# Kernel optimization log

Measured on AMD Instinct MI355X. Metric: run time of the kernel, lower is better.

Reference implementation:

```python
import jax, jax.numpy as jnp
import numpy as np

BATCH = 262144
NUM_LAYERS = 64


def setup_inputs() -> dict:
    key = jax.random.key(0)
    k1, k2, k3 = jax.random.split(key, 3)
    X = jax.random.normal(k1, (BATCH, 2), dtype=jnp.float32)
    weights = jax.random.normal(k2, (NUM_LAYERS, 3), dtype=jnp.float32)
    biases = jax.random.normal(k3, (NUM_LAYERS, 3), dtype=jnp.float32)
    return {"X": X, "weights": weights, "biases": biases}


def _unitaries(X, weights, biases):
    # Pad data with constant 1 -> [B, 3]
    Xp = jnp.concatenate([X, jnp.ones((X.shape[0], 1), X.dtype)], axis=1)
    # angles[b, k, l] = weights[l, k] * Xp[b, k] + biases[l, k]  -> [B, 3, L]
    angles = Xp[:, :, None] * weights.T[None, :, :] + biases.T[None, :, :]
    phi, theta, omega = angles[:, 0, :], angles[:, 1, :], angles[:, 2, :]  # [B, L]
    ct = jnp.cos(theta / 2)
    st = jnp.sin(theta / 2)
    ppo = (phi + omega) / 2
    pmo = (phi - omega) / 2
    m00 = jnp.exp(-1j * ppo) * ct
    m01 = -jnp.exp(1j * pmo) * st
    m10 = jnp.exp(-1j * pmo) * st
    m11 = jnp.exp(1j * ppo) * ct
    # [B, L, 2, 2] -> [L, B, 2, 2]
    M = jnp.stack([jnp.stack([m00, m01], axis=-1),
                   jnp.stack([m10, m11], axis=-1)], axis=-2)
    return jnp.transpose(M, (1, 0, 2, 3))


def reference(X, weights, biases):
    M = _unitaries(X, weights, biases)  # [L, B, 2, 2] complex64
    B = X.shape[0]
    s0 = jnp.tile(jnp.array([1.0 + 0.0j, 0.0 + 0.0j], dtype=M.dtype), (B, 1))  # |0>

    def step(s, u):  # s: [B, 2], u: [B, 2, 2]
        s = jnp.einsum('bij,bj->bi', u, s)
        return s, s

    _, states = jax.lax.scan(step, s0, M)  # [L, B, 2] complex64
    return states
```

## Files before the change

kernel.cpp:

```cpp
#include <hip/hip_runtime.h>

#define BATCH 262144
#define NUM_LAYERS 64

template <int MODE>
__global__ __launch_bounds__(256) void squbit_kernel(
    const float* __restrict__ X,
    const float* __restrict__ W,
    const float* __restrict__ Bi,
    float* __restrict__ out)
{
    __shared__ float4 c4[NUM_LAYERS];
    __shared__ float  com[NUM_LAYERS];

    const int t = threadIdx.x;
    if (t < NUM_LAYERS) {
        const float w0 = W[t * 3 + 0], w1 = W[t * 3 + 1], w2 = W[t * 3 + 2];
        const float b0 = Bi[t * 3 + 0], b1 = Bi[t * 3 + 1], b2 = Bi[t * 3 + 2];
        c4[t]  = make_float4(0.5f * w0, 0.5f * b0, 0.5f * w1, 0.5f * b1);
        com[t] = 0.5f * (w2 + b2);
    }
    __syncthreads();

    const int b = blockIdx.x * 256 + t;
    const float2 x = *reinterpret_cast<const float2*>(X + 2 * b);

    float s0r = 1.0f, s0i = 0.0f, s1r = 0.0f, s1i = 0.0f;

    float2* o2 = reinterpret_cast<float2*>(out) + b;
    float4* o4 = reinterpret_cast<float4*>(out) + b;

    #pragma unroll 4
    for (int l = 0; l < NUM_LAYERS; ++l) {
        const float4 c  = c4[l];
        const float omh = com[l];

        const float ph  = fmaf(x.x, c.x, c.y);
        const float th  = fmaf(x.y, c.z, c.w);
        const float ppo = ph + omh;
        const float pmo = ph - omh;

        float st, ct, sp, cp, sm, cm;
        __sincosf(th,  &st, &ct);
        __sincosf(ppo, &sp, &cp);
        __sincosf(pmo, &sm, &cm);

        const float m00r =  ct * cp, m00i = -ct * sp;
        const float m01r = -st * cm, m01i = -st * sm;
        const float m10r =  st * cm, m10i = -st * sm;
        const float m11r =  ct * cp, m11i =  ct * sp;

        const float n0r = m00r * s0r - m00i * s0i + m01r * s1r - m01i * s1i;
        const float n0i = m00r * s0i + m00i * s0r + m01r * s1i + m01i * s1r;
        const float n1r = m10r * s0r - m10i * s0i + m11r * s1r - m11i * s1i;
        const float n1i = m10r * s0i + m10i * s0r + m11r * s1i + m11i * s1r;

        s0r = n0r; s0i = n0i; s1r = n1r; s1i = n1i;

        if (MODE == 0) {
            o2[l * BATCH] = make_float2(s0r, s1r);
        } else {
            o4[l * BATCH] = make_float4(s0r, s0i, s1r, s1i);
        }
    }
}

extern "C" void kernel_launch(void* const* d_in, const int* in_sizes, int n_in,
                              void* d_out, int out_size, void* d_ws, size_t ws_size,
                              hipStream_t stream) {
    const float* X  = (const float*)d_in[0];
    const float* W  = (const float*)d_in[1];
    const float* Bi = (const float*)d_in[2];
    float* out = (float*)d_out;

    dim3 grid(BATCH / 256), block(256);

    const long long full_complex_floats = (long long)NUM_LAYERS * BATCH * 4;
    if ((long long)out_size >= full_complex_floats) {
        squbit_kernel<1><<<grid, block, 0, stream>>>(X, W, Bi, out);
    } else {
        squbit_kernel<0><<<grid, block, 0, stream>>>(X, W, Bi, out);
    }
}
```

Baseline: 31.55 us.

## Factor unitary into Rz-Ry-Rz, defer omega phase, process two samples per thread

Rewrites each layer's unitary as Rz(omega)·Ry(theta)·Rz(phi) and folds each layer's trailing omega rotation into the next layer's phi angle. The per-batch sincos count drops from three to two, and the omega rotation becomes a constant sincos computed once per block and applied only when writing the output. Each thread now handles two batch elements, with the grid halved, to add instruction-level parallelism and use wider float4 loads and stores. The cost is higher register pressure, and the folded angle could change floating-point rounding slightly.

Result: faster. 29.04 us (-8.0%).

```diff
diff --git a/kernel.cpp b/kernel.cpp
--- a/kernel.cpp
+++ b/kernel.cpp
@@ -10,57 +10,84 @@
     const float* __restrict__ Bi,
     float* __restrict__ out)
 {
-    __shared__ float4 c4[NUM_LAYERS];
-    __shared__ float  com[NUM_LAYERS];
+    __shared__ float4 cA[NUM_LAYERS];
+    __shared__ float2 cOm[NUM_LAYERS];
 
     const int t = threadIdx.x;
     if (t < NUM_LAYERS) {
         const float w0 = W[t * 3 + 0], w1 = W[t * 3 + 1], w2 = W[t * 3 + 2];
         const float b0 = Bi[t * 3 + 0], b1 = Bi[t * 3 + 1], b2 = Bi[t * 3 + 2];
-        c4[t]  = make_float4(0.5f * w0, 0.5f * b0, 0.5f * w1, 0.5f * b1);
-        com[t] = 0.5f * (w2 + b2);
+        float hom_prev = 0.0f;
+        if (t > 0) hom_prev = 0.5f * (W[(t - 1) * 3 + 2] + Bi[(t - 1) * 3 + 2]);
+        cA[t] = make_float4(0.5f * w0, fmaf(0.5f, b0, hom_prev), 0.5f * w1, 0.5f * b1);
+        const float hom = 0.5f * (w2 + b2);
+        float so, co;
+        __sincosf(hom, &so, &co);
+        cOm[t] = make_float2(co, so);
     }
     __syncthreads();
 
-    const int b = blockIdx.x * 256 + t;
-    const float2 x = *reinterpret_cast<const float2*>(X + 2 * b);
+    const int g = blockIdx.x * 256 + t;
+    const float4 xx = reinterpret_cast<const float4*>(X)[g];
 
-    float s0r = 1.0f, s0i = 0.0f, s1r = 0.0f, s1i = 0.0f;
+    float Aur0 = 1.0f, Aui0 = 0.0f, Aur1 = 0.0f, Aui1 = 0.0f;
+    float Bur0 = 1.0f, Bui0 = 0.0f, Bur1 = 0.0f, Bui1 = 0.0f;
 
-    float2* o2 = reinterpret_cast<float2*>(out) + b;
-    float4* o4 = reinterpret_cast<float4*>(out) + b;
+    float4* o4 = reinterpret_cast<float4*>(out);
 
     #pragma unroll 4
     for (int l = 0; l < NUM_LAYERS; ++l) {
-        const float4 c  = c4[l];
-        const float omh = com[l];
+        const float4 c = cA[l];
+        const float2 om = cOm[l];
 
-        const float ph  = fmaf(x.x, c.x, c.y);
-        const float th  = fmaf(x.y, c.z, c.w);
-        const float ppo = ph + omh;
-        const float pmo = ph - omh;
-
-        float st, ct, sp, cp, sm, cm;
-        __sincosf(th,  &st, &ct);
-        __sincosf(ppo, &sp, &cp);
-        __sincosf(pmo, &sm, &cm);
-
-        const float m00r =  ct * cp, m00i = -ct * sp;
-        const float m01r = -st * cm, m01i = -st * sm;
-        const float m10r =  st * cm, m10i = -st * sm;
-        const float m11r =  ct * cp, m11i =  ct * sp;
-
-        const float n0r = m00r * s0r - m00i * s0i + m01r * s1r - m01i * s1i;
-        const float n0i = m00r * s0i + m00i * s0r + m01r * s1i + m01i * s1r;
-        const float n1r = m10r * s0r - m10i * s0i + m11r * s1r - m11i * s1i;
-        const float n1i = m10r * s0i + m10i * s0r + m11r * s1i + m11i * s1r;
-
-        s0r = n0r; s0i = n0i; s1r = n1r; s1i = n1i;
+        {
+            const float hpsi = fmaf(xx.x, c.x, c.y);
+            const float hth  = fmaf(xx.y, c.z, c.w);
+            float sps, cps, sth, cth;
+            __sincosf(hpsi, &sps, &cps);
+            __sincosf(hth,  &sth, &cth);
+            const float a0r = fmaf(Aui0,  sps, Aur0 * cps);
+            const float a0i = fmaf(Aur0, -sps, Aui0 * cps);
+            const float a1r = fmaf(Aui1, -sps, Aur1 * cps);
+            const float a1i = fmaf(Aur1,  sps, Aui1 * cps);
+            Aur0 = fmaf(-sth, a1r, cth * a0r);
+            Aui0 = fmaf(-sth, a1i, cth * a0i);
+            Aur1 = fmaf( sth, a0r, cth * a1r);
+            Aui1 = fmaf( sth, a0i, cth * a1i);
+        }
+        {
+            const float hpsi = fmaf(xx.z, c.x, c.y);
+            const float hth  = fmaf(xx.w, c.z, c.w);
+            float sps, cps, sth, cth;
+            __sincosf(hpsi, &sps, &cps);
+            __sincosf(hth,  &sth, &cth);
+            const float a0r = fmaf(Bui0,  sps, Bur0 * cps);
+            const float a0i = fmaf(Bur0, -sps, Bui0 * cps);
+            const float a1r = fmaf(Bui1, -sps, Bur1 * cps);
+            const float a1i = fmaf(Bur1,  sps, Bui1 * cps);
+            Bur0 = fmaf(-sth, a1r, cth * a0r);
+            Bui0 = fmaf(-sth, a1i, cth * a0i);
+            Bur1 = fmaf( sth, a0r, cth * a1r);
+            Bui1 = fmaf( sth, a0i, cth * a1i);
+        }
 
         if (MODE == 0) {
-            o2[l * BATCH] = make_float2(s0r, s1r);
+            const float At0r = fmaf(Aui0,  om.y, Aur0 * om.x);
+            const float At1r = fmaf(Aui1, -om.y, Aur1 * om.x);
+            const float Bt0r = fmaf(Bui0,  om.y, Bur0 * om.x);
+            const float Bt1r = fmaf(Bui1, -om.y, Bur1 * om.x);
+            o4[l * (BATCH / 2) + g] = make_float4(At0r, At1r, Bt0r, Bt1r);
         } else {
-            o4[l * BATCH] = make_float4(s0r, s0i, s1r, s1i);
+            const float At0r = fmaf(Aui0,  om.y, Aur0 * om.x);
+            const float At0i = fmaf(Aur0, -om.y, Aui0 * om.x);
+            const float At1r = fmaf(Aui1, -om.y, Aur1 * om.x);
+            const float At1i = fmaf(Aur1,  om.y, Aui1 * om.x);
+            const float Bt0r = fmaf(Bui0,  om.y, Bur0 * om.x);
+            const float Bt0i = fmaf(Bur0, -om.y, Bui0 * om.x);
+            const float Bt1r = fmaf(Bui1, -om.y, Bur1 * om.x);
+            const float Bt1i = fmaf(Bur1,  om.y, Bui1 * om.x);
+            o4[(l * BATCH + 2 * g) + 0] = make_float4(At0r, At0i, At1r, At1i);
+            o4[(l * BATCH + 2 * g) + 1] = make_float4(Bt0r, Bt0i, Bt1r, Bt1i);
         }
     }
 }
@@ -73,7 +100,7 @@
     const float* Bi = (const float*)d_in[2];
     float* out = (float*)d_out;
 
-    dim3 grid(BATCH / 256), block(256);
+    dim3 grid(BATCH / 512), block(256);
 
     const long long full_complex_floats = (long long)NUM_LAYERS * BATCH * 4;
     if ((long long)out_size >= full_complex_floats) {
```

## Factor unitaries into Rz/Ry phases, fold omega across layers, two samples per thread

Applied to the files above, without the earlier changes.

Each unitary is rewritten as a product of phase rotations, with the omega rotation of one layer folded into the next layer's phi bias. This cuts the per-sample sincos calls from three to two. The trailing omega phase is applied only to the stored output, using precomputed cos and sin values. Each thread now processes two batch elements with packed float2 vector math and wider stores, and the grid is halved. The risk is a different floating-point rounding path and lower thread-level parallelism.

Result: faster. 26.80 us (-15.0%).

```diff
diff --git a/kernel.cpp b/kernel.cpp
--- a/kernel.cpp
+++ b/kernel.cpp
@@ -2,6 +2,9 @@
 
 #define BATCH 262144
 #define NUM_LAYERS 64
+
+typedef float f32x2 __attribute__((ext_vector_type(2)));
+typedef float f32x4 __attribute__((ext_vector_type(4)));
 
 template <int MODE>
 __global__ __launch_bounds__(256) void squbit_kernel(
@@ -10,57 +13,73 @@
     const float* __restrict__ Bi,
     float* __restrict__ out)
 {
-    __shared__ float4 c4[NUM_LAYERS];
-    __shared__ float  com[NUM_LAYERS];
+    __shared__ float4 cA[NUM_LAYERS];
+    __shared__ float2 cOm[NUM_LAYERS];
 
     const int t = threadIdx.x;
     if (t < NUM_LAYERS) {
         const float w0 = W[t * 3 + 0], w1 = W[t * 3 + 1], w2 = W[t * 3 + 2];
         const float b0 = Bi[t * 3 + 0], b1 = Bi[t * 3 + 1], b2 = Bi[t * 3 + 2];
-        c4[t]  = make_float4(0.5f * w0, 0.5f * b0, 0.5f * w1, 0.5f * b1);
-        com[t] = 0.5f * (w2 + b2);
+        float hom_prev = 0.0f;
+        if (t > 0) hom_prev = 0.5f * (W[(t - 1) * 3 + 2] + Bi[(t - 1) * 3 + 2]);
+        cA[t] = make_float4(0.5f * w0, fmaf(0.5f, b0, hom_prev), 0.5f * w1, 0.5f * b1);
+        const float hom = 0.5f * (w2 + b2);
+        float so, co;
+        __sincosf(hom, &so, &co);
+        cOm[t] = make_float2(co, so);
     }
     __syncthreads();
 
-    const int b = blockIdx.x * 256 + t;
-    const float2 x = *reinterpret_cast<const float2*>(X + 2 * b);
+    const int g = blockIdx.x * 256 + t;
+    const float4 xx = reinterpret_cast<const float4*>(X)[g];
 
-    float s0r = 1.0f, s0i = 0.0f, s1r = 0.0f, s1i = 0.0f;
+    const f32x2 x0 = {xx.x, xx.z};
+    const f32x2 x1 = {xx.y, xx.w};
 
-    float2* o2 = reinterpret_cast<float2*>(out) + b;
-    float4* o4 = reinterpret_cast<float4*>(out) + b;
+    f32x2 ur0 = {1.0f, 1.0f}, ui0 = {0.0f, 0.0f};
+    f32x2 ur1 = {0.0f, 0.0f}, ui1 = {0.0f, 0.0f};
+
+    f32x4* o4 = reinterpret_cast<f32x4*>(out);
 
     #pragma unroll 4
     for (int l = 0; l < NUM_LAYERS; ++l) {
-        const float4 c  = c4[l];
-        const float omh = com[l];
+        const float4 c = cA[l];
+        const float2 om = cOm[l];
 
-        const float ph  = fmaf(x.x, c.x, c.y);
-        const float th  = fmaf(x.y, c.z, c.w);
-        const float ppo = ph + omh;
-        const float pmo = ph - omh;
+        const f32x2 hpsi = x0 * c.x + c.y;
+        const f32x2 hth  = x1 * c.z + c.w;
 
-        float st, ct, sp, cp, sm, cm;
-        __sincosf(th,  &st, &ct);
-        __sincosf(ppo, &sp, &cp);
-        __sincosf(pmo, &sm, &cm);
+        float sps0, cps0, sps1, cps1, sth0, cth0, sth1, cth1;
+        __sincosf(hpsi.x, &sps0, &cps0);
+        __sincosf(hpsi.y, &sps1, &cps1);
+        __sincosf(hth.x,  &sth0, &cth0);
+        __sincosf(hth.y,  &sth1, &cth1);
+        const f32x2 sps = {sps0, sps1}, cps = {cps0, cps1};
+        const f32x2 sth = {sth0, sth1}, cth = {cth0, cth1};
 
-        const float m00r =  ct * cp, m00i = -ct * sp;
-        const float m01r = -st * cm, m01i = -st * sm;
-        const float m10r =  st * cm, m10i = -st * sm;
-        const float m11r =  ct * cp, m11i =  ct * sp;
-
-        const float n0r = m00r * s0r - m00i * s0i + m01r * s1r - m01i * s1i;
-        const float n0i = m00r * s0i + m00i * s0r + m01r * s1i + m01i * s1r;
-        const float n1r = m10r * s0r - m10i * s0i + m11r * s1r - m11i * s1i;
-        const float n1i = m10r * s0i + m10i * s0r + m11r * s1i + m11i * s1r;
-
-        s0r = n0r; s0i = n0i; s1r = n1r; s1i = n1i;
+        const f32x2 a0r = ui0 * sps + ur0 * cps;
+        const f32x2 a0i = ui0 * cps - ur0 * sps;
+        const f32x2 a1r = ur1 * cps - ui1 * sps;
+        const f32x2 a1i = ui1 * cps + ur1 * sps;
+        ur0 = cth * a0r - sth * a1r;
+        ui0 = cth * a0i - sth * a1i;
+        ur1 = sth * a0r + cth * a1r;
+        ui1 = sth * a0i + cth * a1i;
 
         if (MODE == 0) {
-            o2[l * BATCH] = make_float2(s0r, s1r);
+            const f32x2 t0r = ui0 * om.y + ur0 * om.x;
+            const f32x2 t1r = ur1 * om.x - ui1 * om.y;
+            f32x4 v; v.x = t0r.x; v.y = t1r.x; v.z = t0r.y; v.w = t1r.y;
+            o4[l * (BATCH / 2) + g] = v;
         } else {
-            o4[l * BATCH] = make_float4(s0r, s0i, s1r, s1i);
+            const f32x2 t0r = ui0 * om.y + ur0 * om.x;
+            const f32x2 t0i = ui0 * om.x - ur0 * om.y;
+            const f32x2 t1r = ur1 * om.x - ui1 * om.y;
+            const f32x2 t1i = ui1 * om.x + ur1 * om.y;
+            f32x4 va; va.x = t0r.x; va.y = t0i.x; va.z = t1r.x; va.w = t1i.x;
+            f32x4 vb; vb.x = t0r.y; vb.y = t0i.y; vb.z = t1r.y; vb.w = t1i.y;
+            o4[(l * BATCH + 2 * g) + 0] = va;
+            o4[(l * BATCH + 2 * g) + 1] = vb;
         }
     }
 }
@@ -73,7 +92,7 @@
     const float* Bi = (const float*)d_in[2];
     float* out = (float*)d_out;
 
-    dim3 grid(BATCH / 256), block(256);
+    dim3 grid(BATCH / 512), block(256);
 
     const long long full_complex_floats = (long long)NUM_LAYERS * BATCH * 4;
     if ((long long)out_size >= full_complex_floats) {
```
